# Optimization experiments

Measured on AMD Instinct MI355X. Metric: run time of the kernel, lower is better.

## Reference

```python
import jax, jax.numpy as jnp
import numpy as np

F = 64      # input_v_size
E = 64      # emb_v_size
H = 8       # int(sqrt(emb_v_size))
P = 512     # proj_e_size
B, T = 64, 256


def setup_inputs() -> dict:
    key = jax.random.key(0)
    ks = jax.random.split(key, 14)
    s1 = 1.0            # Linear(1->H): fan_in=1
    s2 = 1.0 / np.sqrt(H)
    s3 = 1.0 / np.sqrt(F * E)
    return {
        "x":    jax.random.normal(ks[0], (B, T, F), dtype=jnp.float32),
        "time": jax.random.uniform(ks[1], (B, T, F), dtype=jnp.float32),
        # stacked per-feature Linear(1->H): weight [F,H], bias [F,H]
        "w1v": jax.random.uniform(ks[2], (F, H), jnp.float32, -s1, s1),
        "b1v": jax.random.uniform(ks[3], (F, H), jnp.float32, -s1, s1),
        # stacked per-feature Linear(H->E, bias=False): [F,H,E]
        "w2v": jax.random.uniform(ks[4], (F, H, E), jnp.float32, -s2, s2),
        "w1t": jax.random.uniform(ks[5], (F, H), jnp.float32, -s1, s1),
        "b1t": jax.random.uniform(ks[6], (F, H), jnp.float32, -s1, s1),
        "w2t": jax.random.uniform(ks[7], (F, H, E), jnp.float32, -s2, s2),
        # Wx, Wt: Linear(F*E -> P) stored as [F*E, P] (= torch weight.T)
        "wx":  jax.random.uniform(ks[8], (F * E, P), jnp.float32, -s3, s3),
        "bx":  jax.random.uniform(ks[9], (P,), jnp.float32, -s3, s3),
        "wt":  jax.random.uniform(ks[10], (F * E, P), jnp.float32, -s3, s3),
        "bt":  jax.random.uniform(ks[11], (P,), jnp.float32, -s3, s3),
    }


def _branch(inp, w1, b1, w2):
    # inp [B,T,F]; w1,b1 [F,H]; w2 [F,H,E]
    h = jnp.tanh(inp[..., None] * w1 + b1)          # [B,T,F,H]
    e = jnp.einsum("btfh,fhe->btfe", h, w2)          # [B,T,F,E]
    return e.reshape(*inp.shape[:2], -1)              # [B,T,F*E]


def reference(x, time, w1v, b1v, w2v, w1t, b1t, w2t, wx, bx, wt, bt):
    x_out = _branch(x, w1v, b1v, w2v)
    t_out = _branch(time, w1t, b1t, w2t)
    return (x_out @ wx + bx) + (t_out @ wt + bt)      # [B,T,P]
```

## Files before the change

kernel.cpp:

```cpp
#include <hip/hip_runtime.h>
#include <cstdint>
#include <cstddef>

#define FF 64
#define EE 64
#define HH 8
#define PP 512
#define MM 16384
#define KK 1024

typedef __bf16 bf16x8 __attribute__((ext_vector_type(8)));
typedef float  floatx4 __attribute__((ext_vector_type(4)));

__device__ __forceinline__ unsigned short f2bf(float f) {
    unsigned int u = __float_as_uint(f);
    u += 0x7FFFu + ((u >> 16) & 1u);
    return (unsigned short)(u >> 16);
}

__device__ __forceinline__ unsigned pack2(unsigned short a, unsigned short b) {
    return (unsigned)a | ((unsigned)b << 16);
}

__device__ __forceinline__ float fast_tanh_s(float t) {
    float e, r;
    asm("v_exp_f32 %0, %1" : "=v"(e) : "v"(t));
    float d = e + 1.0f;
    asm("v_rcp_f32 %0, %1" : "=v"(r) : "v"(d));
    return __builtin_fmaf(-2.0f, r, 1.0f);
}

__device__ __forceinline__ void gl_lds16(const unsigned short* g, unsigned short* s) {
    __builtin_amdgcn_global_load_lds(
        (__attribute__((address_space(1))) void*)(void*)g,
        (__attribute__((address_space(3))) void*)s,
        16, 0, 0);
}

__global__ __launch_bounds__(256) void combine_kernel(
    const float* __restrict__ w2v, const float* __restrict__ w2t,
    const float* __restrict__ wx,  const float* __restrict__ wt,
    unsigned short* __restrict__ BmatT)
{
    const int tid = threadIdx.x;
    const int bid = blockIdx.x;
    const int br = bid >> 7;
    const int f  = (bid >> 1) & 63;
    const int nh = bid & 1;
    const float* __restrict__ w2 = br ? w2t : w2v;
    const float* __restrict__ W  = br ? wt  : wx;
    __shared__ float w2s[HH * EE];
    for (int i = tid; i < HH * EE; i += 256) w2s[i] = w2[f * HH * EE + i];
    __syncthreads();
    const int n = nh * 256 + tid;
    float acc[HH] = {0,0,0,0,0,0,0,0};
    const float* Wcol = W + (size_t)f * EE * PP + n;
    #pragma unroll 8
    for (int e = 0; e < EE; ++e) {
        const float wv = Wcol[(size_t)e * PP];
        #pragma unroll
        for (int h = 0; h < HH; ++h)
            acc[h] = __builtin_fmaf(w2s[h * EE + e], wv, acc[h]);
    }
    uint4 v;
    v.x = pack2(f2bf(acc[0]), f2bf(acc[1]));
    v.y = pack2(f2bf(acc[2]), f2bf(acc[3]));
    v.z = pack2(f2bf(acc[4]), f2bf(acc[5]));
    v.w = pack2(f2bf(acc[6]), f2bf(acc[7]));
    *reinterpret_cast<uint4*>(&BmatT[(size_t)n * KK + br * 512 + f * 8]) = v;
}

__global__ __launch_bounds__(256, 3) void gemm_fused_kernel(
    const float* __restrict__ x,   const float* __restrict__ tmv,
    const float* __restrict__ w1v, const float* __restrict__ b1v,
    const float* __restrict__ w1t, const float* __restrict__ b1t,
    const unsigned short* __restrict__ Bt,
    const float* __restrict__ bx, const float* __restrict__ bt,
    float* __restrict__ out)
{
    __shared__ __align__(16) unsigned short As[64 * 64];
    __shared__ __align__(16) unsigned short Bs[256 * 64];
    __shared__ __align__(16) float w1s[2 * FF * HH];
    __shared__ __align__(16) float b1s[2 * FF * HH];

    const int tid  = threadIdx.x;
    const int wave = tid >> 6;
    const int lane = tid & 63;
    const int m0 = blockIdx.x * 64;
    const int n0 = blockIdx.y * 256;

    {
        const float c = 2.8853900817779268f;
        const float4 wsrc = (tid < 128) ? reinterpret_cast<const float4*>(w1v)[tid]
                                        : reinterpret_cast<const float4*>(w1t)[tid - 128];
        const float4 bsrc = (tid < 128) ? reinterpret_cast<const float4*>(b1v)[tid]
                                        : reinterpret_cast<const float4*>(b1t)[tid - 128];
        float4 ws, bs;
        ws.x = wsrc.x * c; ws.y = wsrc.y * c; ws.z = wsrc.z * c; ws.w = wsrc.w * c;
        bs.x = bsrc.x * c; bs.y = bsrc.y * c; bs.z = bsrc.z * c; bs.w = bsrc.w * c;
        reinterpret_cast<float4*>(w1s)[tid] = ws;
        reinterpret_cast<float4*>(b1s)[tid] = bs;
    }

    const int wn  = wave;
    const int q   = lane >> 4;
    const int ml  = lane & 15;
    const int mlx = ml & 7;
    const int lr  = lane >> 3;
    const int lkg = ((lane & 7) ^ lr) * 8;
    const int fi  = tid & 7;
    const int g   = tid >> 3;
    const int pchunkA = (fi ^ (g & 7)) * 8;

    __syncthreads();

    float4 wlo, whi, blo, bhi;
    float  va, vb;
    uint4  pa, pb;

    {
        wlo = reinterpret_cast<const float4*>(w1s)[fi * 2];
        whi = reinterpret_cast<const float4*>(w1s)[fi * 2 + 1];
        blo = reinterpret_cast<const float4*>(b1s)[fi * 2];
        bhi = reinterpret_cast<const float4*>(b1s)[fi * 2 + 1];
        va = x[(size_t)(m0 + g) * FF + fi];
        vb = x[(size_t)(m0 + g + 32) * FF + fi];
    }

    auto tanh_pack = [&](float val) -> uint4 {
        float hv[8];
        hv[0] = fast_tanh_s(__builtin_fmaf(val, wlo.x, blo.x));
        hv[1] = fast_tanh_s(__builtin_fmaf(val, wlo.y, blo.y));
        hv[2] = fast_tanh_s(__builtin_fmaf(val, wlo.z, blo.z));
        hv[3] = fast_tanh_s(__builtin_fmaf(val, wlo.w, blo.w));
        hv[4] = fast_tanh_s(__builtin_fmaf(val, whi.x, bhi.x));
        hv[5] = fast_tanh_s(__builtin_fmaf(val, whi.y, bhi.y));
        hv[6] = fast_tanh_s(__builtin_fmaf(val, whi.z, bhi.z));
        hv[7] = fast_tanh_s(__builtin_fmaf(val, whi.w, bhi.w));
        uint4 v;
        v.x = pack2(f2bf(hv[0]), f2bf(hv[1]));
        v.y = pack2(f2bf(hv[2]), f2bf(hv[3]));
        v.z = pack2(f2bf(hv[4]), f2bf(hv[5]));
        v.w = pack2(f2bf(hv[6]), f2bf(hv[7]));
        return v;
    };
    pa = tanh_pack(va);
    pb = tanh_pack(vb);

    floatx4 acc[4][4];
    #pragma unroll
    for (int i = 0; i < 4; ++i)
        #pragma unroll
        for (int j = 0; j < 4; ++j)
            acc[i][j] = (floatx4){0.f, 0.f, 0.f, 0.f};

    for (int it = 0; it < 16; ++it) {
        const int k0 = it * 64;

        #pragma unroll
        for (int i = 0; i < 8; ++i) {
            const int seg = wave * 8 + i;
            gl_lds16(&Bt[(size_t)(n0 + seg * 8 + lr) * KK + k0 + lkg], &Bs[seg * 512]);
        }
        *reinterpret_cast<uint4*>(&As[g * 64 + pchunkA])        = pa;
        *reinterpret_cast<uint4*>(&As[(g + 32) * 64 + pchunkA]) = pb;

        const int itn = (it < 15) ? it + 1 : 15;
        const int brn = itn >> 3;
        const int fn  = ((itn & 7) << 3) + fi;
        const float* __restrict__ inpn = brn ? tmv : x;
        const float nva = inpn[(size_t)(m0 + g) * FF + fn];
        const float nvb = inpn[(size_t)(m0 + g + 32) * FF + fn];
        const float4 nwlo = reinterpret_cast<const float4*>(w1s)[brn * 128 + fn * 2];
        const float4 nwhi = reinterpret_cast<const float4*>(w1s)[brn * 128 + fn * 2 + 1];
        const float4 nblo = reinterpret_cast<const float4*>(b1s)[brn * 128 + fn * 2];
        const float4 nbhi = reinterpret_cast<const float4*>(b1s)[brn * 128 + fn * 2 + 1];

        __syncthreads();

        wlo = nwlo; whi = nwhi; blo = nblo; bhi = nbhi;
        va = nva; vb = nvb;

        {
            const int co0 = ((0 + q) ^ mlx) * 8;
            bf16x8 af[4], bfr[4];
            #pragma unroll
            for (int mt = 0; mt < 4; ++mt)
                af[mt] = *reinterpret_cast<const bf16x8*>(&As[(mt * 16 + ml) * 64 + co0]);
            #pragma unroll
            for (int nt = 0; nt < 4; ++nt)
                bfr[nt] = *reinterpret_cast<const bf16x8*>(
                    &Bs[(wn * 64 + nt * 16 + ml) * 64 + co0]);
            #pragma unroll
            for (int mt = 0; mt < 4; ++mt)
                #pragma unroll
                for (int nt = 0; nt < 4; ++nt)
                    acc[mt][nt] = __builtin_amdgcn_mfma_f32_16x16x32_bf16(
                        af[mt], bfr[nt], acc[mt][nt], 0, 0, 0);

            pa = tanh_pack(va);
            pb = tanh_pack(vb);

            const int co1 = ((4 + q) ^ mlx) * 8;
            #pragma unroll
            for (int mt = 0; mt < 4; ++mt)
                af[mt] = *reinterpret_cast<const bf16x8*>(&As[(mt * 16 + ml) * 64 + co1]);
            #pragma unroll
            for (int nt = 0; nt < 4; ++nt)
                bfr[nt] = *reinterpret_cast<const bf16x8*>(
                    &Bs[(wn * 64 + nt * 16 + ml) * 64 + co1]);
            #pragma unroll
            for (int mt = 0; mt < 4; ++mt)
                #pragma unroll
                for (int nt = 0; nt < 4; ++nt)
                    acc[mt][nt] = __builtin_amdgcn_mfma_f32_16x16x32_bf16(
                        af[mt], bfr[nt], acc[mt][nt], 0, 0, 0);
        }
        __syncthreads();
    }

    float bias[4];
    #pragma unroll
    for (int nt = 0; nt < 4; ++nt) {
        const int n = n0 + wn * 64 + nt * 16 + ml;
        bias[nt] = bx[n] + bt[n];
    }
    #pragma unroll
    for (int mt = 0; mt < 4; ++mt) {
        const int mb = m0 + mt * 16 + q * 4;
        #pragma unroll
        for (int r = 0; r < 4; ++r) {
            float* orow = out + (size_t)(mb + r) * PP + n0 + wn * 64 + ml;
            #pragma unroll
            for (int nt = 0; nt < 4; ++nt)
                orow[nt * 16] = acc[mt][nt][r] + bias[nt];
        }
    }
}

extern "C" void kernel_launch(void* const* d_in, const int* in_sizes, int n_in,
                              void* d_out, int out_size, void* d_ws, size_t ws_size,
                              hipStream_t stream)
{
    const float* x   = (const float*)d_in[0];
    const float* tmv = (const float*)d_in[1];
    const float* w1v = (const float*)d_in[2];
    const float* b1v = (const float*)d_in[3];
    const float* w2v = (const float*)d_in[4];
    const float* w1t = (const float*)d_in[5];
    const float* b1t = (const float*)d_in[6];
    const float* w2t = (const float*)d_in[7];
    const float* wx  = (const float*)d_in[8];
    const float* bx  = (const float*)d_in[9];
    const float* wt  = (const float*)d_in[10];
    const float* bt  = (const float*)d_in[11];
    float* out = (float*)d_out;

    unsigned short* Bws = (unsigned short*)d_ws;

    combine_kernel<<<256, 256, 0, stream>>>(w2v, w2t, wx, wt, Bws);
    gemm_fused_kernel<<<dim3(MM / 64, PP / 256), 256, 0, stream>>>(
        x, tmv, w1v, b1v, w1t, b1t, Bws, bx, bt, out);
}
```

Measured before the change: 126.5 us.

## Load B fragments directly from global into registers, dropping LDS staging

Drops the shared-memory B tile and its global_load_lds fills. Each wave now reads its own bf16 B fragments straight from global memory into registers for both k-halves of each iteration. Since waves never shared B columns, this removes LDS writes and reads plus the LDS footprint, and the launch-bounds occupancy hint drops from 3 to 2 blocks. In exchange, global load latency is exposed each iteration with no prefetch, and each access is a strided 16-byte read per lane across rows.

```diff
diff --git a/kernel.cpp b/kernel.cpp
--- a/kernel.cpp
+++ b/kernel.cpp
@@ -28,13 +28,6 @@
     float d = e + 1.0f;
     asm("v_rcp_f32 %0, %1" : "=v"(r) : "v"(d));
     return __builtin_fmaf(-2.0f, r, 1.0f);
-}
-
-__device__ __forceinline__ void gl_lds16(const unsigned short* g, unsigned short* s) {
-    __builtin_amdgcn_global_load_lds(
-        (__attribute__((address_space(1))) void*)(void*)g,
-        (__attribute__((address_space(3))) void*)s,
-        16, 0, 0);
 }
 
 __global__ __launch_bounds__(256) void combine_kernel(
@@ -70,7 +63,7 @@
     *reinterpret_cast<uint4*>(&BmatT[(size_t)n * KK + br * 512 + f * 8]) = v;
 }
 
-__global__ __launch_bounds__(256, 3) void gemm_fused_kernel(
+__global__ __launch_bounds__(256, 2) void gemm_fused_kernel(
     const float* __restrict__ x,   const float* __restrict__ tmv,
     const float* __restrict__ w1v, const float* __restrict__ b1v,
     const float* __restrict__ w1t, const float* __restrict__ b1t,
@@ -79,7 +72,6 @@
     float* __restrict__ out)
 {
     __shared__ __align__(16) unsigned short As[64 * 64];
-    __shared__ __align__(16) unsigned short Bs[256 * 64];
     __shared__ __align__(16) float w1s[2 * FF * HH];
     __shared__ __align__(16) float b1s[2 * FF * HH];
 
@@ -106,26 +98,24 @@
     const int q   = lane >> 4;
     const int ml  = lane & 15;
     const int mlx = ml & 7;
-    const int lr  = lane >> 3;
-    const int lkg = ((lane & 7) ^ lr) * 8;
     const int fi  = tid & 7;
     const int g   = tid >> 3;
     const int pchunkA = (fi ^ (g & 7)) * 8;
 
+    const unsigned short* BtL = Bt + (size_t)(n0 + wn * 64 + ml) * KK + q * 8;
+
     __syncthreads();
 
     float4 wlo, whi, blo, bhi;
     float  va, vb;
     uint4  pa, pb;
 
-    {
-        wlo = reinterpret_cast<const float4*>(w1s)[fi * 2];
-        whi = reinterpret_cast<const float4*>(w1s)[fi * 2 + 1];
-        blo = reinterpret_cast<const float4*>(b1s)[fi * 2];
-        bhi = reinterpret_cast<const float4*>(b1s)[fi * 2 + 1];
-        va = x[(size_t)(m0 + g) * FF + fi];
-        vb = x[(size_t)(m0 + g + 32) * FF + fi];
-    }
+    wlo = reinterpret_cast<const float4*>(w1s)[fi * 2];
+    whi = reinterpret_cast<const float4*>(w1s)[fi * 2 + 1];
+    blo = reinterpret_cast<const float4*>(b1s)[fi * 2];
+    bhi = reinterpret_cast<const float4*>(b1s)[fi * 2 + 1];
+    va = x[(size_t)(m0 + g) * FF + fi];
+    vb = x[(size_t)(m0 + g + 32) * FF + fi];
 
     auto tanh_pack = [&](float val) -> uint4 {
         float hv[8];
@@ -157,13 +147,9 @@
     for (int it = 0; it < 16; ++it) {
         const int k0 = it * 64;
 
-        #pragma unroll
-        for (int i = 0; i < 8; ++i) {
-            const int seg = wave * 8 + i;
-            gl_lds16(&Bt[(size_t)(n0 + seg * 8 + lr) * KK + k0 + lkg], &Bs[seg * 512]);
-        }
         *reinterpret_cast<uint4*>(&As[g * 64 + pchunkA])        = pa;
         *reinterpret_cast<uint4*>(&As[(g + 32) * 64 + pchunkA]) = pb;
+        __syncthreads();
 
         const int itn = (it < 15) ? it + 1 : 15;
         const int brn = itn >> 3;
@@ -176,28 +162,29 @@
         const float4 nblo = reinterpret_cast<const float4*>(b1s)[brn * 128 + fn * 2];
         const float4 nbhi = reinterpret_cast<const float4*>(b1s)[brn * 128 + fn * 2 + 1];
 
-        __syncthreads();
-
-        wlo = nwlo; whi = nwhi; blo = nblo; bhi = nbhi;
-        va = nva; vb = nvb;
+        bf16x8 bfr0[4], bfr1[4];
+        #pragma unroll
+        for (int nt = 0; nt < 4; ++nt)
+            bfr0[nt] = *reinterpret_cast<const bf16x8*>(&BtL[(size_t)nt * 16 * KK + k0]);
+        #pragma unroll
+        for (int nt = 0; nt < 4; ++nt)
+            bfr1[nt] = *reinterpret_cast<const bf16x8*>(&BtL[(size_t)nt * 16 * KK + k0 + 32]);
 
         {
             const int co0 = ((0 + q) ^ mlx) * 8;
-            bf16x8 af[4], bfr[4];
+            bf16x8 af[4];
             #pragma unroll
             for (int mt = 0; mt < 4; ++mt)
                 af[mt] = *reinterpret_cast<const bf16x8*>(&As[(mt * 16 + ml) * 64 + co0]);
-            #pragma unroll
-            for (int nt = 0; nt < 4; ++nt)
-                bfr[nt] = *reinterpret_cast<const bf16x8*>(
-                    &Bs[(wn * 64 + nt * 16 + ml) * 64 + co0]);
             #pragma unroll
             for (int mt = 0; mt < 4; ++mt)
                 #pragma unroll
                 for (int nt = 0; nt < 4; ++nt)
                     acc[mt][nt] = __builtin_amdgcn_mfma_f32_16x16x32_bf16(
-                        af[mt], bfr[nt], acc[mt][nt], 0, 0, 0);
-
+                        af[mt], bfr0[nt], acc[mt][nt], 0, 0, 0);
+
+            wlo = nwlo; whi = nwhi; blo = nblo; bhi = nbhi;
+            va = nva; vb = nvb;
             pa = tanh_pack(va);
             pb = tanh_pack(vb);
 
@@ -205,16 +192,12 @@
             #pragma unroll
             for (int mt = 0; mt < 4; ++mt)
                 af[mt] = *reinterpret_cast<const bf16x8*>(&As[(mt * 16 + ml) * 64 + co1]);
-            #pragma unroll
-            for (int nt = 0; nt < 4; ++nt)
-                bfr[nt] = *reinterpret_cast<const bf16x8*>(
-                    &Bs[(wn * 64 + nt * 16 + ml) * 64 + co1]);
             #pragma unroll
             for (int mt = 0; mt < 4; ++mt)
                 #pragma unroll
                 for (int nt = 0; nt < 4; ++nt)
                     acc[mt][nt] = __builtin_amdgcn_mfma_f32_16x16x32_bf16(
-                        af[mt], bfr[nt], acc[mt][nt], 0, 0, 0);
+                        af[mt], bfr1[nt], acc[mt][nt], 0, 0, 0);
         }
         __syncthreads();
     }
```

Result: slower. 145.2 us (+14.8%).

## Double-buffer B tiles with K=32 steps and prefetch next tile during MFMA

Applied to the files above, without the earlier changes.

Restructures the fused GEMM main loop from 16 iterations of K=64 into 32 iterations of K=32, with a double-buffered B tile in shared memory. The load for the next B tile is issued before the current tile is computed, and a partial vmcnt wait plus a raw barrier replaces __syncthreads. The aim is to overlap global-to-LDS transfer with MFMA work. Occupancy hint drops from 3 to 2 blocks per SM, and the new swizzle and the inline-asm waitcnt count must exactly match the number of outstanding loads to stay correct.

```diff
diff --git a/kernel.cpp b/kernel.cpp
--- a/kernel.cpp
+++ b/kernel.cpp
@@ -70,7 +70,7 @@
     *reinterpret_cast<uint4*>(&BmatT[(size_t)n * KK + br * 512 + f * 8]) = v;
 }
 
-__global__ __launch_bounds__(256, 3) void gemm_fused_kernel(
+__global__ __launch_bounds__(256, 2) void gemm_fused_kernel(
     const float* __restrict__ x,   const float* __restrict__ tmv,
     const float* __restrict__ w1v, const float* __restrict__ b1v,
     const float* __restrict__ w1t, const float* __restrict__ b1t,
@@ -78,8 +78,8 @@
     const float* __restrict__ bx, const float* __restrict__ bt,
     float* __restrict__ out)
 {
-    __shared__ __align__(16) unsigned short As[64 * 64];
-    __shared__ __align__(16) unsigned short Bs[256 * 64];
+    __shared__ __align__(16) unsigned short Bs[2 * 256 * 32];
+    __shared__ __align__(16) unsigned short As[64 * 32];
     __shared__ __align__(16) float w1s[2 * FF * HH];
     __shared__ __align__(16) float b1s[2 * FF * HH];
 
@@ -105,27 +105,18 @@
     const int wn  = wave;
     const int q   = lane >> 4;
     const int ml  = lane & 15;
-    const int mlx = ml & 7;
-    const int lr  = lane >> 3;
-    const int lkg = ((lane & 7) ^ lr) * 8;
-    const int fi  = tid & 7;
-    const int g   = tid >> 3;
-    const int pchunkA = (fi ^ (g & 7)) * 8;
+    const int fco = ((q + (ml >> 1)) & 3) * 8;
+    const int fi2  = tid & 3;
+    const int arow = tid >> 2;
+    const int asoff = arow * 32 + ((fi2 + (arow >> 1)) & 3) * 8;
+    const int laneClog = ((lane & 3) - ((lane >> 3) & 3)) & 3;
+    const unsigned short* BtLane =
+        Bt + (size_t)(n0 + (lane >> 2)) * KK + laneClog * 8;
 
     __syncthreads();
 
     float4 wlo, whi, blo, bhi;
-    float  va, vb;
-    uint4  pa, pb;
-
-    {
-        wlo = reinterpret_cast<const float4*>(w1s)[fi * 2];
-        whi = reinterpret_cast<const float4*>(w1s)[fi * 2 + 1];
-        blo = reinterpret_cast<const float4*>(b1s)[fi * 2];
-        bhi = reinterpret_cast<const float4*>(b1s)[fi * 2 + 1];
-        va = x[(size_t)(m0 + g) * FF + fi];
-        vb = x[(size_t)(m0 + g + 32) * FF + fi];
-    }
+    uint4  pa;
 
     auto tanh_pack = [&](float val) -> uint4 {
         float hv[8];
@@ -144,8 +135,18 @@
         v.w = pack2(f2bf(hv[6]), f2bf(hv[7]));
         return v;
     };
-    pa = tanh_pack(va);
-    pb = tanh_pack(vb);
+
+    const float val0 = x[(size_t)(m0 + arow) * FF + fi2];
+    #pragma unroll
+    for (int i = 0; i < 4; ++i) {
+        const int seg = wave * 4 + i;
+        gl_lds16(BtLane + (size_t)seg * 16 * KK, &Bs[seg * 512]);
+    }
+    wlo = reinterpret_cast<const float4*>(w1s)[fi2 * 2];
+    whi = reinterpret_cast<const float4*>(w1s)[fi2 * 2 + 1];
+    blo = reinterpret_cast<const float4*>(b1s)[fi2 * 2];
+    bhi = reinterpret_cast<const float4*>(b1s)[fi2 * 2 + 1];
+    pa = tanh_pack(val0);
 
     floatx4 acc[4][4];
     #pragma unroll
@@ -154,43 +155,43 @@
         for (int j = 0; j < 4; ++j)
             acc[i][j] = (floatx4){0.f, 0.f, 0.f, 0.f};
 
-    for (int it = 0; it < 16; ++it) {
-        const int k0 = it * 64;
-
-        #pragma unroll
-        for (int i = 0; i < 8; ++i) {
-            const int seg = wave * 8 + i;
-            gl_lds16(&Bt[(size_t)(n0 + seg * 8 + lr) * KK + k0 + lkg], &Bs[seg * 512]);
+    for (int it = 0; it < 32; ++it) {
+        const int buf = it & 1;
+        const int itn = (it < 31) ? it + 1 : 31;
+        const int brn = itn >> 4;
+        const int fn  = ((itn & 15) << 2) + fi2;
+
+        const float* __restrict__ inpn = brn ? tmv : x;
+        const float nval = inpn[(size_t)(m0 + arow) * FF + fn];
+
+        {
+            unsigned short* BsN = &Bs[(buf ^ 1) * (256 * 32)];
+            const unsigned short* src = BtLane + (size_t)itn * 32;
+            #pragma unroll
+            for (int i = 0; i < 4; ++i) {
+                const int seg = wave * 4 + i;
+                gl_lds16(src + (size_t)seg * 16 * KK, BsN + seg * 512);
+            }
         }
-        *reinterpret_cast<uint4*>(&As[g * 64 + pchunkA])        = pa;
-        *reinterpret_cast<uint4*>(&As[(g + 32) * 64 + pchunkA]) = pb;
-
-        const int itn = (it < 15) ? it + 1 : 15;
-        const int brn = itn >> 3;
-        const int fn  = ((itn & 7) << 3) + fi;
-        const float* __restrict__ inpn = brn ? tmv : x;
-        const float nva = inpn[(size_t)(m0 + g) * FF + fn];
-        const float nvb = inpn[(size_t)(m0 + g + 32) * FF + fn];
+
+        *reinterpret_cast<uint4*>(&As[asoff]) = pa;
         const float4 nwlo = reinterpret_cast<const float4*>(w1s)[brn * 128 + fn * 2];
         const float4 nwhi = reinterpret_cast<const float4*>(w1s)[brn * 128 + fn * 2 + 1];
         const float4 nblo = reinterpret_cast<const float4*>(b1s)[brn * 128 + fn * 2];
         const float4 nbhi = reinterpret_cast<const float4*>(b1s)[brn * 128 + fn * 2 + 1];
 
-        __syncthreads();
-
-        wlo = nwlo; whi = nwhi; blo = nblo; bhi = nbhi;
-        va = nva; vb = nvb;
+        asm volatile("s_waitcnt vmcnt(5) lgkmcnt(0)\n\ts_barrier" ::: "memory");
 
         {
-            const int co0 = ((0 + q) ^ mlx) * 8;
+            const unsigned short* BsC = &Bs[buf * (256 * 32)];
             bf16x8 af[4], bfr[4];
             #pragma unroll
             for (int mt = 0; mt < 4; ++mt)
-                af[mt] = *reinterpret_cast<const bf16x8*>(&As[(mt * 16 + ml) * 64 + co0]);
+                af[mt] = *reinterpret_cast<const bf16x8*>(&As[(mt * 16 + ml) * 32 + fco]);
             #pragma unroll
             for (int nt = 0; nt < 4; ++nt)
                 bfr[nt] = *reinterpret_cast<const bf16x8*>(
-                    &Bs[(wn * 64 + nt * 16 + ml) * 64 + co0]);
+                    &BsC[(wn * 64 + nt * 16 + ml) * 32 + fco]);
             #pragma unroll
             for (int mt = 0; mt < 4; ++mt)
                 #pragma unroll
@@ -198,25 +199,11 @@
                     acc[mt][nt] = __builtin_amdgcn_mfma_f32_16x16x32_bf16(
                         af[mt], bfr[nt], acc[mt][nt], 0, 0, 0);
 
-            pa = tanh_pack(va);
-            pb = tanh_pack(vb);
-
-            const int co1 = ((4 + q) ^ mlx) * 8;
-            #pragma unroll
-            for (int mt = 0; mt < 4; ++mt)
-                af[mt] = *reinterpret_cast<const bf16x8*>(&As[(mt * 16 + ml) * 64 + co1]);
-            #pragma unroll
-            for (int nt = 0; nt < 4; ++nt)
-                bfr[nt] = *reinterpret_cast<const bf16x8*>(
-                    &Bs[(wn * 64 + nt * 16 + ml) * 64 + co1]);
-            #pragma unroll
-            for (int mt = 0; mt < 4; ++mt)
-                #pragma unroll
-                for (int nt = 0; nt < 4; ++nt)
-                    acc[mt][nt] = __builtin_amdgcn_mfma_f32_16x16x32_bf16(
-                        af[mt], bfr[nt], acc[mt][nt], 0, 0, 0);
+            wlo = nwlo; whi = nwhi; blo = nblo; bhi = nbhi;
+            pa = tanh_pack(nval);
         }
-        __syncthreads();
+
+        asm volatile("s_waitcnt lgkmcnt(0)\n\ts_barrier" ::: "memory");
     }
 
     float bias[4];
```

After: 129.5 us. 2.4% more time.
